# Kernel tuning notes

Measured on AMD Instinct MI355X. Metric: run time of the kernel, lower is better.

Reference implementation:

```python
import jax, jax.numpy as jnp
import numpy as np

C = 256
DK = C // 8  # query/key channels


def setup_inputs() -> dict:
    key = jax.random.key(0)
    ks = jax.random.split(key, 7)
    B, W, H = 4, 64, 64
    x = jax.random.normal(ks[0], (B, C, W, H), dtype=jnp.float32)
    s_in = 1.0 / np.sqrt(C)
    Wq = jax.random.normal(ks[1], (DK, C), dtype=jnp.float32) * s_in
    bq = jnp.zeros((DK,), dtype=jnp.float32)
    Wk = jax.random.normal(ks[2], (DK, C), dtype=jnp.float32) * s_in
    bk = jnp.zeros((DK,), dtype=jnp.float32)
    Wv = jax.random.normal(ks[3], (C, C), dtype=jnp.float32) * s_in
    bv = jnp.zeros((C,), dtype=jnp.float32)
    return {"x": x, "Wq": Wq, "bq": bq, "Wk": Wk, "bk": bk, "Wv": Wv, "bv": bv}


def reference(x, Wq, bq, Wk, bk, Wv, bv):
    B, Cc, W, H = x.shape
    N = W * H
    xf = x.reshape(B, Cc, N)  # (B, C, N) flattened spatial
    # 1x1 convs == channel matmuls
    q = jnp.einsum('dc,bcn->bnd', Wq, xf) + bq  # (B, N, DK)
    k = jnp.einsum('dc,bcn->bdn', Wk, xf) + bk[None, :, None]  # (B, DK, N)
    v = jnp.einsum('oc,bcn->bon', Wv, xf) + bv[None, :, None]  # (B, C, N)
    energy = jnp.einsum('bnd,bdm->bnm', q, k) / jnp.sqrt(jnp.float32(q.shape[-1]))
    attn = jax.nn.softmax(energy, axis=-1)  # (B, N, N)
    out = jnp.einsum('bcn,bmn->bcm', v, attn)  # v @ attn^T
    return out.reshape(B, Cc, W, H) + x
```

## Files before the change

kernel.cpp:

```cpp
#include <hip/hip_runtime.h>
#include <hip/hip_bf16.h>
#include <math.h>

#define BB 4
#define CC 256
#define DKK 32
#define NN 4096
#define QSCALE2 0.25503489022324213f

typedef __attribute__((ext_vector_type(8))) __bf16 bf16x8;
typedef __attribute__((ext_vector_type(4))) __bf16 bf16x4;
typedef __attribute__((ext_vector_type(4))) float f32x4;
typedef __attribute__((ext_vector_type(16))) float f32x16;

#define XROW 264

__global__ __launch_bounds__(256) void qkv2_kernel(
    const float* __restrict__ x,
    const float* __restrict__ Wq, const float* __restrict__ Wk,
    const float* __restrict__ Wv,
    const float* __restrict__ bq, const float* __restrict__ bk,
    const float* __restrict__ bv,
    __bf16* __restrict__ qws, __bf16* __restrict__ kws, __bf16* __restrict__ vws)
{
    __shared__ __align__(16) unsigned char smemB[32 * XROW * 2];
    __bf16* xs = (__bf16*)smemB;
    float (*scr)[33] = (float (*)[33])smemB;

    const int tid = threadIdx.x;
    const int w   = tid >> 6;
    const int l   = tid & 63;
    const int l15 = l & 15;
    const int lq  = l >> 4;
    const int n0  = blockIdx.x * 32;
    const int b   = blockIdx.y;

    {
        const int cl = tid >> 3;
        const int nf = (tid & 7) * 4;
#pragma unroll
        for (int p = 0; p < 8; p++) {
            int c = p * 32 + cl;
            float4 v = *(const float4*)&x[((size_t)(b * CC + c)) * NN + n0 + nf];
            xs[(nf + 0) * XROW + c] = (__bf16)v.x;
            xs[(nf + 1) * XROW + c] = (__bf16)v.y;
            xs[(nf + 2) * XROW + c] = (__bf16)v.z;
            xs[(nf + 3) * XROW + c] = (__bf16)v.w;
        }
    }

    const float* wrow[5];
#pragma unroll
    for (int ot = 0; ot < 5; ot++) {
        int ob = 80 * w + ot * 16;
        const float* mat; int r0;
        if (ob < 32)      { mat = Wq; r0 = ob; }
        else if (ob < 64) { mat = Wk; r0 = ob - 32; }
        else              { mat = Wv; r0 = ob - 64; }
        wrow[ot] = mat + (size_t)(r0 + l15) * CC + lq * 8;
    }

    __syncthreads();

    const f32x4 zf = {0.f, 0.f, 0.f, 0.f};
    f32x4 acc[5][2];
#pragma unroll
    for (int i = 0; i < 5; i++)
#pragma unroll
        for (int j = 0; j < 2; j++) acc[i][j] = zf;

    const __bf16* xls = &xs[l15 * XROW + lq * 8];

    bf16x8 bcur[2], acur[5], bnxt[2], anxt[5];
#pragma unroll
    for (int nt = 0; nt < 2; nt++) bcur[nt] = *(const bf16x8*)(xls + nt * 16 * XROW);
#pragma unroll
    for (int ot = 0; ot < 5; ot++) {
        f32x4 a0 = *(const f32x4*)(wrow[ot]);
        f32x4 a1 = *(const f32x4*)(wrow[ot] + 4);
        bf16x8 af;
#pragma unroll
        for (int j = 0; j < 4; j++) { af[j] = (__bf16)a0[j]; af[4 + j] = (__bf16)a1[j]; }
        acur[ot] = af;
    }

#pragma unroll
    for (int ks = 0; ks < 8; ks++) {
        if (ks < 7) {
#pragma unroll
            for (int nt = 0; nt < 2; nt++)
                bnxt[nt] = *(const bf16x8*)(xls + nt * 16 * XROW + (ks + 1) * 32);
#pragma unroll
            for (int ot = 0; ot < 5; ot++) {
                f32x4 a0 = *(const f32x4*)(wrow[ot] + (ks + 1) * 32);
                f32x4 a1 = *(const f32x4*)(wrow[ot] + (ks + 1) * 32 + 4);
                bf16x8 af;
#pragma unroll
                for (int j = 0; j < 4; j++) { af[j] = (__bf16)a0[j]; af[4 + j] = (__bf16)a1[j]; }
                anxt[ot] = af;
            }
        }
#pragma unroll
        for (int ot = 0; ot < 5; ot++)
#pragma unroll
            for (int nt = 0; nt < 2; nt++)
                acc[ot][nt] = __builtin_amdgcn_mfma_f32_16x16x32_bf16(acur[ot], bcur[nt], acc[ot][nt], 0, 0, 0);
        if (ks < 7) {
#pragma unroll
            for (int nt = 0; nt < 2; nt++) bcur[nt] = bnxt[nt];
#pragma unroll
            for (int ot = 0; ot < 5; ot++) acur[ot] = anxt[ot];
        }
    }

    __syncthreads();

    __bf16* vchunk = vws + (size_t)b * CC * NN + (size_t)(n0 >> 5) * 8192;
#pragma unroll
    for (int ot = 0; ot < 5; ot++) {
        int ob = 80 * w + ot * 16;
#pragma unroll
        for (int nt = 0; nt < 2; nt++) {
#pragma unroll
            for (int r = 0; r < 4; r++) {
                int o = ob + lq * 4 + r;
                int n = nt * 16 + l15;
                float val = acc[ot][nt][r];
                if (ob >= 64) {
                    int c  = o - 64;
                    int ct = c >> 5, c5 = c & 31;
                    vchunk[ct * 1024 + nt * 512 + c5 * 16 + l15] =
                        (__bf16)(val + bv[c]);
                } else if (ob < 32) {
                    scr[o][n] = (val + bq[o]) * QSCALE2;
                } else {
                    scr[o][n] = val + bk[o - 32];
                }
            }
        }
    }
    __syncthreads();
    {
        int n  = tid >> 3;
        int d0 = (tid & 7) * 4;
        bf16x4 qv, kv;
#pragma unroll
        for (int j = 0; j < 4; j++) {
            qv[j] = (__bf16)scr[d0 + j][n];
            kv[j] = (__bf16)scr[32 + d0 + j][n];
        }
        size_t base = ((size_t)b * NN + n0 + n) * DKK + d0;
        *(bf16x4*)&qws[base] = qv;
        *(bf16x4*)&kws[base] = kv;
    }
}

#define PSTD 18
#define PWB  (64 * PSTD * 4)
#define MST 68

__global__ __launch_bounds__(256, 2) void attn_kernel(
    const __bf16* __restrict__ qb, const __bf16* __restrict__ kb,
    const __bf16* __restrict__ vt, const float* __restrict__ x,
    float* __restrict__ out)
{
    __shared__ __align__(16) unsigned char smem[38144];
    const int tid = threadIdx.x;
    const int w   = tid >> 6;
    const int l   = tid & 63;
    const int m31 = l & 31;
    const int hi  = l >> 5;
    const int mx  = m31 & 3;
    unsigned char* pwb = smem + w * 2 * PWB;
    float* Ls   = (float*)(smem + 36864);
    float* Linv = (float*)(smem + 37888);

    const int beta = blockIdx.x;
    const int b    = (beta >> 1) & 3;
    const int ch   = (beta >> 3) & 1;
    const int mt64 = ((beta >> 4) << 1) | (beta & 1);
    const int m0   = mt64 * 64;

    const __bf16* qbb = qb + (size_t)b * NN * DKK;
    const __bf16* kbb = kb + (size_t)b * NN * DKK;
    const __bf16* vtb = vt + (size_t)b * CC * NN;

    bf16x8 qa[2][2];
#pragma unroll
    for (int mt = 0; mt < 2; mt++)
#pragma unroll
        for (int kk = 0; kk < 2; kk++)
            qa[mt][kk] = *(const bf16x8*)(qbb + (size_t)(m0 + mt * 32 + m31) * DKK + kk * 16 + hi * 8);

    const __bf16* kstrip = kbb + (size_t)(w * 32 + m31) * DKK + hi * 8;
    const __bf16* vstrip = vtb + (size_t)w * 8192 + (size_t)ch * 4096
                               + m31 * 16 + hi * 8;

    const f32x16 zf16 = {0.f,0.f,0.f,0.f,0.f,0.f,0.f,0.f,
                         0.f,0.f,0.f,0.f,0.f,0.f,0.f,0.f};
    f32x16 acc[4][2];
#pragma unroll
    for (int ct = 0; ct < 4; ct++)
#pragma unroll
        for (int mt = 0; mt < 2; mt++) acc[ct][mt] = zf16;
    float lacc[2] = {0.f, 0.f};

    auto kq_step = [&](int bufoff, bf16x8 kA0, bf16x8 kA1) {
#pragma unroll
        for (int mt = 0; mt < 2; mt++) {
            f32x16 e = __builtin_amdgcn_mfma_f32_32x32x16_bf16(kA0, qa[mt][0], zf16, 0, 0, 0);
            e = __builtin_amdgcn_mfma_f32_32x32x16_bf16(kA1, qa[mt][1], e, 0, 0, 0);
            float s = 0.f;
#pragma unroll
            for (int g = 0; g < 4; g++) {
                bf16x4 pb;
#pragma unroll
                for (int t = 0; t < 4; t++) {
                    float v = __builtin_amdgcn_exp2f(e[4 * g + t]);
                    s += v; pb[t] = (__bf16)v;
                }
                *(bf16x4*)(pwb + bufoff + (mt * 32 + m31) * 72 + ((g ^ mx) * 16 + hi * 8)) = pb;
            }
            lacc[mt] += s;
        }
    };

    union PU { bf16x8 v; bf16x4 h[2]; };
    auto pf_read = [&](int bufoff, bf16x8 (&pf)[2][2]) {
#pragma unroll
        for (int mt = 0; mt < 2; mt++)
#pragma unroll
            for (int kk = 0; kk < 2; kk++) {
                int sb = (((kk * 2 + hi) ^ mx) * 16);
                PU u;
                u.h[0] = *(const bf16x4*)(pwb + bufoff + (mt * 32 + m31) * 72 + sb);
                u.h[1] = *(const bf16x4*)(pwb + bufoff + (mt * 32 + m31) * 72 + sb + 8);
                pf[mt][kk] = u.v;
            }
    };

    {
        bf16x8 kA0 = *(const bf16x8*)kstrip;
        bf16x8 kA1 = *(const bf16x8*)(kstrip + 16);
        kq_step(0, kA0, kA1);
    }
    bf16x8 kA0 = *(const bf16x8*)(kstrip + (size_t)128 * DKK);
    bf16x8 kA1 = *(const bf16x8*)(kstrip + (size_t)128 * DKK + 16);

#pragma unroll 2
    for (int ic = 0; ic < 31; ic++) {
        const int cur = ic & 1;
        const __bf16* vch = vstrip + (size_t)ic * 32768;

        bf16x8 vA[4], vB[4];
#pragma unroll
        for (int ct = 0; ct < 4; ct++)
            vA[ct] = *(const bf16x8*)(vch + ct * 1024);

        bf16x8 pf[2][2];
        pf_read(cur * PWB, pf);

        kq_step((cur ^ 1) * PWB, kA0, kA1);

#pragma unroll
        for (int ct = 0; ct < 4; ct++)
            vB[ct] = *(const bf16x8*)(vch + ct * 1024 + 512);

        kA0 = *(const bf16x8*)(kstrip + (size_t)(ic + 2) * 128 * DKK);
        kA1 = *(const bf16x8*)(kstrip + (size_t)(ic + 2) * 128 * DKK + 16);

        __builtin_amdgcn_s_setprio(1);
#pragma unroll
        for (int ct = 0; ct < 4; ct++)
#pragma unroll
            for (int mt = 0; mt < 2; mt++) {
                acc[ct][mt] = __builtin_amdgcn_mfma_f32_32x32x16_bf16(vA[ct], pf[mt][0], acc[ct][mt], 0, 0, 0);
                acc[ct][mt] = __builtin_amdgcn_mfma_f32_32x32x16_bf16(vB[ct], pf[mt][1], acc[ct][mt], 0, 0, 0);
            }
        __builtin_amdgcn_s_setprio(0);
    }

    {
        const __bf16* vch = vstrip + (size_t)31 * 32768;
        bf16x8 pf[2][2];
        pf_read(PWB, pf);
        bf16x8 vA[4], vB[4];
#pragma unroll
        for (int ct = 0; ct < 4; ct++) vA[ct] = *(const bf16x8*)(vch + ct * 1024);
#pragma unroll
        for (int ct = 0; ct < 4; ct++) vB[ct] = *(const bf16x8*)(vch + ct * 1024 + 512);
        __builtin_amdgcn_s_setprio(1);
#pragma unroll
        for (int ct = 0; ct < 4; ct++)
#pragma unroll
            for (int mt = 0; mt < 2; mt++) {
                acc[ct][mt] = __builtin_amdgcn_mfma_f32_32x32x16_bf16(vA[ct], pf[mt][0], acc[ct][mt], 0, 0, 0);
                acc[ct][mt] = __builtin_amdgcn_mfma_f32_32x32x16_bf16(vB[ct], pf[mt][1], acc[ct][mt], 0, 0, 0);
            }
        __builtin_amdgcn_s_setprio(0);
    }

#pragma unroll
    for (int mt = 0; mt < 2; mt++) lacc[mt] += __shfl_xor(lacc[mt], 32, 64);
    if (hi == 0) {
#pragma unroll
        for (int mt = 0; mt < 2; mt++) Ls[w * 64 + mt * 32 + m31] = lacc[mt];
    }
    __syncthreads();
    if (tid < 64)
        Linv[tid] = 1.0f / (Ls[tid] + Ls[64 + tid] + Ls[128 + tid] + Ls[192 + tid]);

    float* Ored = (float*)smem + w * (32 * MST);
#pragma unroll
    for (int q = 0; q < 4; q++) {
        if (q > 0) __syncthreads();
#pragma unroll
        for (int mt = 0; mt < 2; mt++)
#pragma unroll
            for (int reg = 0; reg < 16; reg++) {
                int crow = (reg & 3) + 8 * (reg >> 2) + 4 * hi;
                Ored[crow * MST + mt * 32 + m31] = acc[q][mt][reg];
            }
        __syncthreads();
        const int cl  = tid >> 3;
        const int mi0 = (tid & 7) * 8;
        const float* Ob = (const float*)smem + cl * MST;
#pragma unroll
        for (int j = 0; j < 2; j++) {
            int mi = mi0 + 4 * j;
            f32x4 s = *(const f32x4*)&Ob[mi];
            s = s + *(const f32x4*)&Ob[1 * (32 * MST) + mi];
            s = s + *(const f32x4*)&Ob[2 * (32 * MST) + mi];
            s = s + *(const f32x4*)&Ob[3 * (32 * MST) + mi];
            f32x4 li = *(const f32x4*)&Linv[mi];
            int c = ch * 128 + q * 32 + cl;
            size_t gi = ((size_t)(b * CC + c)) * NN + m0 + mi;
            f32x4 xr = *(const f32x4*)&x[gi];
            *(f32x4*)&out[gi] = s * li + xr;
        }
    }
}

extern "C" void kernel_launch(void* const* d_in, const int* in_sizes, int n_in,
                              void* d_out, int out_size, void* d_ws, size_t ws_size,
                              hipStream_t stream) {
    const float* x  = (const float*)d_in[0];
    const float* Wq = (const float*)d_in[1];
    const float* bq = (const float*)d_in[2];
    const float* Wk = (const float*)d_in[3];
    const float* bk = (const float*)d_in[4];
    const float* Wv = (const float*)d_in[5];
    const float* bv = (const float*)d_in[6];
    float* out = (float*)d_out;

    __bf16* qws = (__bf16*)d_ws;
    __bf16* kws = qws + (size_t)BB * NN * DKK;
    __bf16* vws = kws + (size_t)BB * NN * DKK;

    qkv2_kernel<<<dim3(128, BB), 256, 0, stream>>>(x, Wq, Wk, Wv, bq, bk, bv,
                                                   qws, kws, vws);
    attn_kernel<<<dim3(512), 256, 0, stream>>>(qws, kws, vws, x, out);
}
```

Measured before the change: 150.8 us.

## Transpose softmax probabilities in registers with permlane32_swap instead of LDS

Replaces the per-wave LDS round-trip that converted the exp'd QK^T MFMA output into the B-operand layout for the PV MFMA with in-register permlane32_swap exchanges. This removes LDS writes, reads and the double-buffered staging. With no buffer to stage into, the software pipeline that computed the next chunk's probabilities ahead of the current PV MFMAs is dropped, and the loop now runs all 32 chunks uniformly. LDS use shrinks, but the exp and pack work now sits directly before the dependent MFMAs, which loses some overlap.

New measurement: 156.0 us. 3.5% more time.

```diff
diff --git a/kernel.cpp b/kernel.cpp
--- a/kernel.cpp
+++ b/kernel.cpp
@@ -155,8 +155,6 @@
     }
 }
 
-#define PSTD 18
-#define PWB  (64 * PSTD * 4)
 #define MST 68
 
 __global__ __launch_bounds__(256, 2) void attn_kernel(
@@ -164,16 +162,14 @@
     const __bf16* __restrict__ vt, const float* __restrict__ x,
     float* __restrict__ out)
 {
-    __shared__ __align__(16) unsigned char smem[38144];
+    __shared__ __align__(16) unsigned char smem[36096];
     const int tid = threadIdx.x;
     const int w   = tid >> 6;
     const int l   = tid & 63;
     const int m31 = l & 31;
     const int hi  = l >> 5;
-    const int mx  = m31 & 3;
-    unsigned char* pwb = smem + w * 2 * PWB;
-    float* Ls   = (float*)(smem + 36864);
-    float* Linv = (float*)(smem + 37888);
+    float* Ls   = (float*)(smem + 34816);
+    float* Linv = (float*)(smem + 35840);
 
     const int beta = blockIdx.x;
     const int b    = (beta >> 1) & 3;
@@ -205,90 +201,63 @@
         for (int mt = 0; mt < 2; mt++) acc[ct][mt] = zf16;
     float lacc[2] = {0.f, 0.f};
 
-    auto kq_step = [&](int bufoff, bf16x8 kA0, bf16x8 kA1) {
+    union PU { unsigned u[4]; bf16x8 v; };
+    auto kq_pack = [&](bf16x8 kA0, bf16x8 kA1, bf16x8 (&pf)[2][2]) {
 #pragma unroll
         for (int mt = 0; mt < 2; mt++) {
             f32x16 e = __builtin_amdgcn_mfma_f32_32x32x16_bf16(kA0, qa[mt][0], zf16, 0, 0, 0);
             e = __builtin_amdgcn_mfma_f32_32x32x16_bf16(kA1, qa[mt][1], e, 0, 0, 0);
             float s = 0.f;
-#pragma unroll
-            for (int g = 0; g < 4; g++) {
+            unsigned g[4][2];
+#pragma unroll
+            for (int gi = 0; gi < 4; gi++) {
                 bf16x4 pb;
 #pragma unroll
                 for (int t = 0; t < 4; t++) {
-                    float v = __builtin_amdgcn_exp2f(e[4 * g + t]);
+                    float v = __builtin_amdgcn_exp2f(e[4 * gi + t]);
                     s += v; pb[t] = (__bf16)v;
                 }
-                *(bf16x4*)(pwb + bufoff + (mt * 32 + m31) * 72 + ((g ^ mx) * 16 + hi * 8)) = pb;
+                PU tu; *(bf16x4*)tu.u = pb;
+                g[gi][0] = tu.u[0]; g[gi][1] = tu.u[1];
             }
             lacc[mt] += s;
+#pragma unroll
+            for (int kk = 0; kk < 2; kk++) {
+                PU r;
+#pragma unroll
+                for (int wi = 0; wi < 2; wi++) {
+                    auto sw = __builtin_amdgcn_permlane32_swap(
+                        (int)g[kk * 2][wi], (int)g[kk * 2 + 1][wi], false, false);
+                    r.u[wi]     = (unsigned)sw[0];
+                    r.u[2 + wi] = (unsigned)sw[1];
+                }
+                pf[mt][kk] = r.v;
+            }
         }
     };
 
-    union PU { bf16x8 v; bf16x4 h[2]; };
-    auto pf_read = [&](int bufoff, bf16x8 (&pf)[2][2]) {
-#pragma unroll
-        for (int mt = 0; mt < 2; mt++)
-#pragma unroll
-            for (int kk = 0; kk < 2; kk++) {
-                int sb = (((kk * 2 + hi) ^ mx) * 16);
-                PU u;
-                u.h[0] = *(const bf16x4*)(pwb + bufoff + (mt * 32 + m31) * 72 + sb);
-                u.h[1] = *(const bf16x4*)(pwb + bufoff + (mt * 32 + m31) * 72 + sb + 8);
-                pf[mt][kk] = u.v;
-            }
-    };
-
-    {
-        bf16x8 kA0 = *(const bf16x8*)kstrip;
-        bf16x8 kA1 = *(const bf16x8*)(kstrip + 16);
-        kq_step(0, kA0, kA1);
-    }
-    bf16x8 kA0 = *(const bf16x8*)(kstrip + (size_t)128 * DKK);
-    bf16x8 kA1 = *(const bf16x8*)(kstrip + (size_t)128 * DKK + 16);
-
+    bf16x8 kA0 = *(const bf16x8*)kstrip;
+    bf16x8 kA1 = *(const bf16x8*)(kstrip + 16);
 #pragma unroll 2
-    for (int ic = 0; ic < 31; ic++) {
-        const int cur = ic & 1;
+    for (int ic = 0; ic < 32; ic++) {
         const __bf16* vch = vstrip + (size_t)ic * 32768;
 
-        bf16x8 vA[4], vB[4];
+        bf16x8 vA[4];
 #pragma unroll
         for (int ct = 0; ct < 4; ct++)
             vA[ct] = *(const bf16x8*)(vch + ct * 1024);
 
         bf16x8 pf[2][2];
-        pf_read(cur * PWB, pf);
-
-        kq_step((cur ^ 1) * PWB, kA0, kA1);
-
+        kq_pack(kA0, kA1, pf);
+
+        kA0 = *(const bf16x8*)(kstrip + (size_t)(ic + 1) * 128 * DKK);
+        kA1 = *(const bf16x8*)(kstrip + (size_t)(ic + 1) * 128 * DKK + 16);
+
+        bf16x8 vB[4];
 #pragma unroll
         for (int ct = 0; ct < 4; ct++)
             vB[ct] = *(const bf16x8*)(vch + ct * 1024 + 512);
 
-        kA0 = *(const bf16x8*)(kstrip + (size_t)(ic + 2) * 128 * DKK);
-        kA1 = *(const bf16x8*)(kstrip + (size_t)(ic + 2) * 128 * DKK + 16);
-
-        __builtin_amdgcn_s_setprio(1);
-#pragma unroll
-        for (int ct = 0; ct < 4; ct++)
-#pragma unroll
-            for (int mt = 0; mt < 2; mt++) {
-                acc[ct][mt] = __builtin_amdgcn_mfma_f32_32x32x16_bf16(vA[ct], pf[mt][0], acc[ct][mt], 0, 0, 0);
-                acc[ct][mt] = __builtin_amdgcn_mfma_f32_32x32x16_bf16(vB[ct], pf[mt][1], acc[ct][mt], 0, 0, 0);
-            }
-        __builtin_amdgcn_s_setprio(0);
-    }
-
-    {
-        const __bf16* vch = vstrip + (size_t)31 * 32768;
-        bf16x8 pf[2][2];
-        pf_read(PWB, pf);
-        bf16x8 vA[4], vB[4];
-#pragma unroll
-        for (int ct = 0; ct < 4; ct++) vA[ct] = *(const bf16x8*)(vch + ct * 1024);
-#pragma unroll
-        for (int ct = 0; ct < 4; ct++) vB[ct] = *(const bf16x8*)(vch + ct * 1024 + 512);
         __builtin_amdgcn_s_setprio(1);
 #pragma unroll
         for (int ct = 0; ct < 4; ct++)
```

## Split QKV projection into bf16 transpose prep kernel plus direct-load GEMM

Applied to the files above, without the earlier changes.

Adds a prep kernel that converts x to a transposed bf16 layout (batch, n, c) and converts the stacked Wq/Wk/Wv weights to bf16 once. The QKV kernel then loads MFMA operands straight from global memory without the LDS staging, the per-element fp32-to-bf16 conversion of weights and one barrier. It also splits the softmax row-sum accumulation into independent partial sums to shorten the dependency chain. In exchange it adds a third kernel launch and an extra round trip of x through global memory.

Result: no change. 148.3 us (-1.6%).

```diff
diff --git a/kernel.cpp b/kernel.cpp
--- a/kernel.cpp
+++ b/kernel.cpp
@@ -13,19 +13,61 @@
 typedef __attribute__((ext_vector_type(4))) float f32x4;
 typedef __attribute__((ext_vector_type(16))) float f32x16;
 
-#define XROW 264
-
-__global__ __launch_bounds__(256) void qkv2_kernel(
-    const float* __restrict__ x,
+__global__ __launch_bounds__(256) void prep_kernel(
+    const float* __restrict__ x, __bf16* __restrict__ xT,
     const float* __restrict__ Wq, const float* __restrict__ Wk,
-    const float* __restrict__ Wv,
+    const float* __restrict__ Wv, __bf16* __restrict__ Wb)
+{
+    __shared__ float xs[64][68];
+    const int tid = threadIdx.x;
+    const int n0 = blockIdx.x * 64;
+    const int c0 = blockIdx.y * 64;
+    const int b  = blockIdx.z;
+
+    if (b == 0) {
+        int unit = blockIdx.y * 64 + blockIdx.x;
+        if (unit < 80) {
+            int i = (unit * 256 + tid) * 4;
+            int row = i >> 8, col = i & 255;
+            const float* src;
+            if (row < 32)      src = &Wq[row * 256 + col];
+            else if (row < 64) src = &Wk[(row - 32) * 256 + col];
+            else               src = &Wv[(row - 64) * 256 + col];
+            float4 v = *(const float4*)src;
+            Wb[i]     = (__bf16)v.x;
+            Wb[i + 1] = (__bf16)v.y;
+            Wb[i + 2] = (__bf16)v.z;
+            Wb[i + 3] = (__bf16)v.w;
+        }
+    }
+
+#pragma unroll
+    for (int p = 0; p < 4; p++) {
+        int cc = p * 16 + (tid >> 4);
+        int nf = (tid & 15) * 4;
+        float4 v = *(const float4*)&x[((size_t)(b * CC + c0 + cc)) * NN + n0 + nf];
+        xs[cc][nf] = v.x; xs[cc][nf + 1] = v.y; xs[cc][nf + 2] = v.z; xs[cc][nf + 3] = v.w;
+    }
+    __syncthreads();
+    int n = tid >> 2, cs = (tid & 3) * 16;
+    bf16x8 lo, hi;
+#pragma unroll
+    for (int j = 0; j < 8; j++) {
+        lo[j] = (__bf16)xs[cs + j][n];
+        hi[j] = (__bf16)xs[cs + 8 + j][n];
+    }
+    size_t base = ((size_t)(b * NN + n0 + n)) * CC + c0 + cs;
+    *(bf16x8*)&xT[base]     = lo;
+    *(bf16x8*)&xT[base + 8] = hi;
+}
+
+__global__ __launch_bounds__(256) void qkv_kernel(
+    const __bf16* __restrict__ xT, const __bf16* __restrict__ Wb,
     const float* __restrict__ bq, const float* __restrict__ bk,
     const float* __restrict__ bv,
     __bf16* __restrict__ qws, __bf16* __restrict__ kws, __bf16* __restrict__ vws)
 {
-    __shared__ __align__(16) unsigned char smemB[32 * XROW * 2];
-    __bf16* xs = (__bf16*)smemB;
-    float (*scr)[33] = (float (*)[33])smemB;
+    __shared__ float scr[64][33];
 
     const int tid = threadIdx.x;
     const int w   = tid >> 6;
@@ -35,32 +77,8 @@
     const int n0  = blockIdx.x * 32;
     const int b   = blockIdx.y;
 
-    {
-        const int cl = tid >> 3;
-        const int nf = (tid & 7) * 4;
-#pragma unroll
-        for (int p = 0; p < 8; p++) {
-            int c = p * 32 + cl;
-            float4 v = *(const float4*)&x[((size_t)(b * CC + c)) * NN + n0 + nf];
-            xs[(nf + 0) * XROW + c] = (__bf16)v.x;
-            xs[(nf + 1) * XROW + c] = (__bf16)v.y;
-            xs[(nf + 2) * XROW + c] = (__bf16)v.z;
-            xs[(nf + 3) * XROW + c] = (__bf16)v.w;
-        }
-    }
-
-    const float* wrow[5];
-#pragma unroll
-    for (int ot = 0; ot < 5; ot++) {
-        int ob = 80 * w + ot * 16;
-        const float* mat; int r0;
-        if (ob < 32)      { mat = Wq; r0 = ob; }
-        else if (ob < 64) { mat = Wk; r0 = ob - 32; }
-        else              { mat = Wv; r0 = ob - 64; }
-        wrow[ot] = mat + (size_t)(r0 + l15) * CC + lq * 8;
-    }
-
-    __syncthreads();
+    const __bf16* xbase = xT + ((size_t)b * NN + n0 + l15) * CC + lq * 8;
+    const __bf16* wbase = Wb + (size_t)(80 * w + l15) * CC + lq * 8;
 
     const f32x4 zf = {0.f, 0.f, 0.f, 0.f};
     f32x4 acc[5][2];
@@ -69,36 +87,21 @@
 #pragma unroll
         for (int j = 0; j < 2; j++) acc[i][j] = zf;
 
-    const __bf16* xls = &xs[l15 * XROW + lq * 8];
-
     bf16x8 bcur[2], acur[5], bnxt[2], anxt[5];
 #pragma unroll
-    for (int nt = 0; nt < 2; nt++) bcur[nt] = *(const bf16x8*)(xls + nt * 16 * XROW);
-#pragma unroll
-    for (int ot = 0; ot < 5; ot++) {
-        f32x4 a0 = *(const f32x4*)(wrow[ot]);
-        f32x4 a1 = *(const f32x4*)(wrow[ot] + 4);
-        bf16x8 af;
-#pragma unroll
-        for (int j = 0; j < 4; j++) { af[j] = (__bf16)a0[j]; af[4 + j] = (__bf16)a1[j]; }
-        acur[ot] = af;
-    }
+    for (int nt = 0; nt < 2; nt++) bcur[nt] = *(const bf16x8*)(xbase + nt * 16 * CC);
+#pragma unroll
+    for (int ot = 0; ot < 5; ot++) acur[ot] = *(const bf16x8*)(wbase + ot * 16 * CC);
 
 #pragma unroll
     for (int ks = 0; ks < 8; ks++) {
         if (ks < 7) {
 #pragma unroll
             for (int nt = 0; nt < 2; nt++)
-                bnxt[nt] = *(const bf16x8*)(xls + nt * 16 * XROW + (ks + 1) * 32);
-#pragma unroll
-            for (int ot = 0; ot < 5; ot++) {
-                f32x4 a0 = *(const f32x4*)(wrow[ot] + (ks + 1) * 32);
-                f32x4 a1 = *(const f32x4*)(wrow[ot] + (ks + 1) * 32 + 4);
-                bf16x8 af;
-#pragma unroll
-                for (int j = 0; j < 4; j++) { af[j] = (__bf16)a0[j]; af[4 + j] = (__bf16)a1[j]; }
-                anxt[ot] = af;
-            }
+                bnxt[nt] = *(const bf16x8*)(xbase + nt * 16 * CC + (ks + 1) * 32);
+#pragma unroll
+            for (int ot = 0; ot < 5; ot++)
+                anxt[ot] = *(const bf16x8*)(wbase + ot * 16 * CC + (ks + 1) * 32);
         }
 #pragma unroll
         for (int ot = 0; ot < 5; ot++)
@@ -112,8 +115,6 @@
             for (int ot = 0; ot < 5; ot++) acur[ot] = anxt[ot];
         }
     }
-
-    __syncthreads();
 
     __bf16* vchunk = vws + (size_t)b * CC * NN + (size_t)(n0 >> 5) * 8192;
 #pragma unroll
@@ -210,18 +211,20 @@
         for (int mt = 0; mt < 2; mt++) {
             f32x16 e = __builtin_amdgcn_mfma_f32_32x32x16_bf16(kA0, qa[mt][0], zf16, 0, 0, 0);
             e = __builtin_amdgcn_mfma_f32_32x32x16_bf16(kA1, qa[mt][1], e, 0, 0, 0);
-            float s = 0.f;
+            float sg[4];
 #pragma unroll
             for (int g = 0; g < 4; g++) {
                 bf16x4 pb;
+                float s = 0.f;
 #pragma unroll
                 for (int t = 0; t < 4; t++) {
                     float v = __builtin_amdgcn_exp2f(e[4 * g + t]);
                     s += v; pb[t] = (__bf16)v;
                 }
+                sg[g] = s;
                 *(bf16x4*)(pwb + bufoff + (mt * 32 + m31) * 72 + ((g ^ mx) * 16 + hi * 8)) = pb;
             }
-            lacc[mt] += s;
+            lacc[mt] += (sg[0] + sg[1]) + (sg[2] + sg[3]);
         }
     };
 
@@ -356,8 +359,10 @@
     __bf16* qws = (__bf16*)d_ws;
     __bf16* kws = qws + (size_t)BB * NN * DKK;
     __bf16* vws = kws + (size_t)BB * NN * DKK;
-
-    qkv2_kernel<<<dim3(128, BB), 256, 0, stream>>>(x, Wq, Wk, Wv, bq, bk, bv,
-                                                   qws, kws, vws);
+    __bf16* Wb  = vws + (size_t)BB * CC * NN;
+    __bf16* xT  = Wb  + (size_t)320 * CC;
+
+    prep_kernel<<<dim3(64, 4, BB), 256, 0, stream>>>(x, xT, Wq, Wk, Wv, Wb);
+    qkv_kernel <<<dim3(128, BB), 256, 0, stream>>>(xT, Wb, bq, bk, bv, qws, kws, vws);
     attn_kernel<<<dim3(512), 256, 0, stream>>>(qws, kws, vws, x, out);
 }
```
